# Kernel tuning notes

Hardware: AMD Instinct MI355X
Metric: run time of the kernel (lower is better)

The kernel has to match this reference:

```python
import jax, jax.numpy as jnp
import numpy as np
from jax import lax

Q = 3          # Self-ONN polynomial order
EPS = 1e-5     # InstanceNorm1d eps


def setup_inputs() -> dict:
    key = jax.random.key(0)
    k1, k2, k3 = jax.random.split(key, 3)
    B, Cin, L = 16, 128, 8192
    Cout, K = 128, 3
    x = jax.random.normal(k1, (B, Cin, L), dtype=jnp.float32)
    # Conv1d weight over power-expanded channels: [Cout, Cin*Q, K]
    W = jax.random.normal(k2, (Cout, Cin * Q, K), dtype=jnp.float32) * 0.05
    b = jax.random.normal(k3, (Cout,), dtype=jnp.float32) * 0.05
    return {"x": x, "W": W, "b": b}


def reference(x, W, b):
    x = jnp.repeat(x, 2, axis=-1)
    # Self-ONN power expansion: concat x^1..x^Q along channel dim -> (B, C*Q, 2L)
    powers = jnp.concatenate([x ** (i + 1) for i in range(Q)], axis=1)
    # Conv1d, stride 1, padding 1 (same length)
    out = lax.conv_general_dilated(
        powers, W,
        window_strides=(1,),
        padding=[(1, 1)],
        dimension_numbers=("NCH", "OIH", "NCH"),
    ) + b[None, :, None]
    # InstanceNorm1d (affine=False): normalize over length per (batch, channel)
    mean = jnp.mean(out, axis=-1, keepdims=True)
    var = jnp.var(out, axis=-1, keepdims=True)
    out = (out - mean) * lax.rsqrt(var + EPS)
    # Tanh activation (self.relu is nn.Tanh()); dropout=False -> no-op
    return jnp.tanh(out)
```

## Files before the change

kernel.cpp:

```cpp
#include <hip/hip_runtime.h>
#include <hip/hip_fp16.h>
#include <math.h>

#define BATCH 16
#define CIN   128
#define LIN   8192
#define COUT  128
#define LOUT  16384
#define KEXP  768
#define NT    128
#define NTILES (LIN/NT)
#define PCOLS 130
#define PCPAD 136
#define PSZ   (PCOLS*PCPAD)

typedef _Float16 f16x8 __attribute__((ext_vector_type(8)));
typedef float    f32x4 __attribute__((ext_vector_type(4)));

__global__ void prep_weights(const float* __restrict__ W,
                             _Float16* __restrict__ WE,
                             _Float16* __restrict__ WO) {
  int idx = blockIdx.x * 256 + threadIdx.x;
  int co = idx / KEXP;
  int k  = idx % KEXP;
  int cq = (k < 384) ? k : k - 384;
  const float* w = W + ((size_t)co * 384 + cq) * 3;
  float we, wo;
  if (k < 384) { we = w[0];        wo = w[0] + w[1]; }
  else         { we = w[1] + w[2]; wo = w[2];        }
  int mtile = co >> 4, l15 = co & 15;
  int ks = k >> 5, kk = k & 31, quad = kk >> 3, j = kk & 7;
  size_t off = ((size_t)((mtile * 24 + ks) * 64) + quad * 16 + l15) * 8 + j;
  WE[off] = (_Float16)we;
  WO[off] = (_Float16)wo;
}

__launch_bounds__(512, 2)
__global__ void conv_gemm(const float* __restrict__ x,
                          const _Float16* __restrict__ WE,
                          const _Float16* __restrict__ WO,
                          float* __restrict__ out,
                          float* __restrict__ stats) {
  extern __shared__ char smem[];
  float*    sstats = (float*)smem;
  _Float16* plane  = (_Float16*)(smem + 1024);

  const int tile = blockIdx.x;
  const int b    = blockIdx.y;
  const int i0   = tile * NT;
  const int t    = threadIdx.x;
  const int lane = t & 63;
  const int wave = t >> 6;
  const int p    = wave >> 1;
  const int isO  = wave & 1;
  const int wm   = p >> 1, wn = p & 1;
  const int l15  = lane & 15, quad = lane >> 4;

  if (t < 128) { sstats[2 * t] = 0.f; sstats[2 * t + 1] = 0.f; }

  const float* xb = x + (size_t)b * CIN * LIN;
  for (int task = t; task < PCOLS * 16; task += 512) {
    int g   = task / PCOLS;
    int col = task - g * PCOLS;
    int c8  = g * 8;
    int gi  = i0 - 1 + col;
    bool ok = (gi >= 0 && gi < LIN);
    f16x8 p1, p2, p3;
#pragma unroll
    for (int j = 0; j < 8; ++j) {
      float v = ok ? xb[(size_t)(c8 + j) * LIN + gi] : 0.f;
      float v2 = v * v;
      p1[j] = (_Float16)v;
      p2[j] = (_Float16)v2;
      p3[j] = (_Float16)(v2 * v);
    }
    _Float16* dst = plane + col * PCPAD + c8;
    *(f16x8*)(dst)           = p1;
    *(f16x8*)(dst + PSZ)     = p2;
    *(f16x8*)(dst + 2 * PSZ) = p3;
  }
  __syncthreads();

  f32x4 acc[4][4];
  const f32x4 zero = {0.f, 0.f, 0.f, 0.f};
#pragma unroll
  for (int fm = 0; fm < 4; ++fm)
#pragma unroll
    for (int fn = 0; fn < 4; ++fn) acc[fm][fn] = zero;

  const _Float16* Wsel = isO ? WO : WE;
  const int kl = quad * 8;

  f16x8 af[2][4], bf[2][4];

#define LOAD_STEP(ks_, buf_)                                                        \
  {                                                                                 \
    const int q_  = ((ks_) % 12) >> 2;                                              \
    const int cb_ = ((ks_) & 3) * 32;                                               \
    const int sh_ = ((ks_) < 12 ? 0 : 1) + isO;                                     \
    const _Float16* pb_ = plane + q_ * PSZ + cb_ + kl;                              \
    _Pragma("unroll")                                                               \
    for (int fn = 0; fn < 4; ++fn) {                                                \
      int colB = wn * 64 + fn * 16 + l15 + sh_;                                     \
      bf[buf_][fn] = *(const f16x8*)(pb_ + colB * PCPAD);                           \
    }                                                                               \
    _Pragma("unroll")                                                               \
    for (int fm = 0; fm < 4; ++fm) {                                                \
      int mt = wm * 4 + fm;                                                         \
      af[buf_][fm] = *(const f16x8*)(Wsel + ((size_t)((mt * 24 + (ks_)) * 64) + lane) * 8); \
    }                                                                               \
  }

  LOAD_STEP(0, 0)
#pragma unroll
  for (int ks = 0; ks < 24; ++ks) {
    const int cur = ks & 1, nxt = cur ^ 1;
    if (ks < 23) LOAD_STEP(ks + 1, nxt)
#pragma unroll
    for (int fm = 0; fm < 4; ++fm)
#pragma unroll
      for (int fn = 0; fn < 4; ++fn)
        acc[fm][fn] = __builtin_amdgcn_mfma_f32_16x16x32_f16(af[cur][fm], bf[cur][fn], acc[fm][fn], 0, 0, 0);
  }
#undef LOAD_STEP

  __syncthreads();
  char* ex = smem + 1024 + p * (64 * 272) + lane * 272;
  if (isO) {
#pragma unroll
    for (int fm = 0; fm < 4; ++fm)
#pragma unroll
      for (int fn = 0; fn < 4; ++fn)
        *(f32x4*)(ex + (fm * 4 + fn) * 16) = acc[fm][fn];
  }
  __syncthreads();

  if (!isO) {
    float* orow_base = out + (size_t)b * COUT * LOUT;
#pragma unroll
    for (int fm = 0; fm < 4; ++fm) {
      f32x4 accO[4];
#pragma unroll
      for (int fn = 0; fn < 4; ++fn) accO[fn] = *(f32x4*)(ex + (fm * 4 + fn) * 16);
#pragma unroll
      for (int r = 0; r < 4; ++r) {
        float s1 = 0.f, s2 = 0.f;
#pragma unroll
        for (int fn = 0; fn < 4; ++fn) {
          float vE = acc[fm][fn][r], vO = accO[fn][r];
          s1 += vE + vO;
          s2 += vE * vE + vO * vO;
        }
#pragma unroll
        for (int off = 8; off >= 1; off >>= 1) {
          s1 += __shfl_xor(s1, off, 64);
          s2 += __shfl_xor(s2, off, 64);
        }
        int co = wm * 64 + fm * 16 + quad * 4 + r;
        if (l15 == 0) {
          atomicAdd(&sstats[2 * co], s1);
          atomicAdd(&sstats[2 * co + 1], s2);
        }
        float* orow = orow_base + (size_t)co * LOUT;
#pragma unroll
        for (int fn = 0; fn < 4; ++fn) {
          int n = i0 + wn * 64 + fn * 16 + l15;
          float2 v = make_float2(acc[fm][fn][r], accO[fn][r]);
          *(float2*)(orow + 2 * n) = v;
        }
      }
    }
  }
  __syncthreads();
  if (t < 128) {
    atomicAdd(&stats[((size_t)b * COUT + t) * 2],     sstats[2 * t]);
    atomicAdd(&stats[((size_t)b * COUT + t) * 2 + 1], sstats[2 * t + 1]);
  }
}

__device__ inline float tanh_fast(float z) {
  float e = __expf(2.f * z);
  return 1.f - 2.f / (e + 1.f);
}

__global__ void norm_tanh(float* __restrict__ out, const float* __restrict__ stats) {
  int row = blockIdx.x;
  float s1 = stats[2 * row], s2 = stats[2 * row + 1];
  const float invN = 1.f / (float)LOUT;
  float mean = s1 * invN;
  float var  = fmaxf(s2 * invN - mean * mean, 0.f);
  float inv  = rsqrtf(var + 1e-5f);
  float4* p = (float4*)(out + (size_t)row * LOUT);
  for (int i = threadIdx.x; i < LOUT / 4; i += 256) {
    float4 v = p[i];
    v.x = tanh_fast((v.x - mean) * inv);
    v.y = tanh_fast((v.y - mean) * inv);
    v.z = tanh_fast((v.z - mean) * inv);
    v.w = tanh_fast((v.w - mean) * inv);
    p[i] = v;
  }
}

extern "C" void kernel_launch(void* const* d_in, const int* in_sizes, int n_in,
                              void* d_out, int out_size, void* d_ws, size_t ws_size,
                              hipStream_t stream) {
  const float* x = (const float*)d_in[0];
  const float* W = (const float*)d_in[1];
  float* out = (float*)d_out;

  float*    stats = (float*)d_ws;
  _Float16* WE    = (_Float16*)((char*)d_ws + 16384);
  _Float16* WO    = WE + (size_t)COUT * KEXP;

  hipMemsetAsync(d_ws, 0, 16384, stream);
  prep_weights<<<dim3((COUT * KEXP) / 256), dim3(256), 0, stream>>>(W, WE, WO);

  size_t shmem = 1024 + (size_t)3 * PSZ * 2;
  hipFuncSetAttribute(reinterpret_cast<const void*>(conv_gemm),
                      hipFuncAttributeMaxDynamicSharedMemorySize, (int)shmem);
  conv_gemm<<<dim3(NTILES, BATCH), dim3(512), shmem, stream>>>(x, WE, WO, out, stats);

  norm_tanh<<<dim3(BATCH * COUT), dim3(256), 0, stream>>>(out, stats);
}
```

Measured before the change: 328.5 us.

## Stream power planes one at a time to cut LDS and raise occupancy

```diff
diff --git a/kernel.cpp b/kernel.cpp
--- a/kernel.cpp
+++ b/kernel.cpp
@@ -23,19 +23,23 @@
   int idx = blockIdx.x * 256 + threadIdx.x;
   int co = idx / KEXP;
   int k  = idx % KEXP;
-  int cq = (k < 384) ? k : k - 384;
+  int sh = (k >= 384) ? 1 : 0;
+  int cq = k - 384 * sh;
   const float* w = W + ((size_t)co * 384 + cq) * 3;
   float we, wo;
-  if (k < 384) { we = w[0];        wo = w[0] + w[1]; }
+  if (sh == 0) { we = w[0];        wo = w[0] + w[1]; }
   else         { we = w[1] + w[2]; wo = w[2];        }
+  int q  = cq >> 7;
+  int c  = cq & 127;
+  int ks = q * 8 + sh * 4 + (c >> 5);
+  int kk = c & 31, quad = kk >> 3, j = kk & 7;
   int mtile = co >> 4, l15 = co & 15;
-  int ks = k >> 5, kk = k & 31, quad = kk >> 3, j = kk & 7;
   size_t off = ((size_t)((mtile * 24 + ks) * 64) + quad * 16 + l15) * 8 + j;
   WE[off] = (_Float16)we;
   WO[off] = (_Float16)wo;
 }
 
-__launch_bounds__(512, 2)
+__launch_bounds__(512, 4)
 __global__ void conv_gemm(const float* __restrict__ x,
                           const _Float16* __restrict__ WE,
                           const _Float16* __restrict__ WO,
@@ -55,31 +59,12 @@
   const int isO  = wave & 1;
   const int wm   = p >> 1, wn = p & 1;
   const int l15  = lane & 15, quad = lane >> 4;
+  const int kl   = quad * 8;
 
   if (t < 128) { sstats[2 * t] = 0.f; sstats[2 * t + 1] = 0.f; }
 
   const float* xb = x + (size_t)b * CIN * LIN;
-  for (int task = t; task < PCOLS * 16; task += 512) {
-    int g   = task / PCOLS;
-    int col = task - g * PCOLS;
-    int c8  = g * 8;
-    int gi  = i0 - 1 + col;
-    bool ok = (gi >= 0 && gi < LIN);
-    f16x8 p1, p2, p3;
-#pragma unroll
-    for (int j = 0; j < 8; ++j) {
-      float v = ok ? xb[(size_t)(c8 + j) * LIN + gi] : 0.f;
-      float v2 = v * v;
-      p1[j] = (_Float16)v;
-      p2[j] = (_Float16)v2;
-      p3[j] = (_Float16)(v2 * v);
-    }
-    _Float16* dst = plane + col * PCPAD + c8;
-    *(f16x8*)(dst)           = p1;
-    *(f16x8*)(dst + PSZ)     = p2;
-    *(f16x8*)(dst + 2 * PSZ) = p3;
-  }
-  __syncthreads();
+  const _Float16* Wsel = isO ? WO : WE;
 
   f32x4 acc[4][4];
   const f32x4 zero = {0.f, 0.f, 0.f, 0.f};
@@ -88,86 +73,77 @@
 #pragma unroll
     for (int fn = 0; fn < 4; ++fn) acc[fm][fn] = zero;
 
-  const _Float16* Wsel = isO ? WO : WE;
-  const int kl = quad * 8;
-
-  f16x8 af[2][4], bf[2][4];
-
-#define LOAD_STEP(ks_, buf_)                                                        \
-  {                                                                                 \
-    const int q_  = ((ks_) % 12) >> 2;                                              \
-    const int cb_ = ((ks_) & 3) * 32;                                               \
-    const int sh_ = ((ks_) < 12 ? 0 : 1) + isO;                                     \
-    const _Float16* pb_ = plane + q_ * PSZ + cb_ + kl;                              \
-    _Pragma("unroll")                                                               \
-    for (int fn = 0; fn < 4; ++fn) {                                                \
-      int colB = wn * 64 + fn * 16 + l15 + sh_;                                     \
-      bf[buf_][fn] = *(const f16x8*)(pb_ + colB * PCPAD);                           \
-    }                                                                               \
-    _Pragma("unroll")                                                               \
-    for (int fm = 0; fm < 4; ++fm) {                                                \
-      int mt = wm * 4 + fm;                                                         \
-      af[buf_][fm] = *(const f16x8*)(Wsel + ((size_t)((mt * 24 + (ks_)) * 64) + lane) * 8); \
-    }                                                                               \
-  }
-
-  LOAD_STEP(0, 0)
-#pragma unroll
-  for (int ks = 0; ks < 24; ++ks) {
-    const int cur = ks & 1, nxt = cur ^ 1;
-    if (ks < 23) LOAD_STEP(ks + 1, nxt)
-#pragma unroll
-    for (int fm = 0; fm < 4; ++fm)
-#pragma unroll
-      for (int fn = 0; fn < 4; ++fn)
-        acc[fm][fn] = __builtin_amdgcn_mfma_f32_16x16x32_f16(af[cur][fm], bf[cur][fn], acc[fm][fn], 0, 0, 0);
-  }
-#undef LOAD_STEP
-
-  __syncthreads();
-  char* ex = smem + 1024 + p * (64 * 272) + lane * 272;
-  if (isO) {
-#pragma unroll
-    for (int fm = 0; fm < 4; ++fm)
-#pragma unroll
-      for (int fn = 0; fn < 4; ++fn)
-        *(f32x4*)(ex + (fm * 4 + fn) * 16) = acc[fm][fn];
-  }
-  __syncthreads();
-
-  if (!isO) {
-    float* orow_base = out + (size_t)b * COUT * LOUT;
-#pragma unroll
-    for (int fm = 0; fm < 4; ++fm) {
-      f32x4 accO[4];
-#pragma unroll
-      for (int fn = 0; fn < 4; ++fn) accO[fn] = *(f32x4*)(ex + (fm * 4 + fn) * 16);
-#pragma unroll
-      for (int r = 0; r < 4; ++r) {
-        float s1 = 0.f, s2 = 0.f;
-#pragma unroll
-        for (int fn = 0; fn < 4; ++fn) {
-          float vE = acc[fm][fn][r], vO = accO[fn][r];
-          s1 += vE + vO;
-          s2 += vE * vE + vO * vO;
-        }
-#pragma unroll
-        for (int off = 8; off >= 1; off >>= 1) {
-          s1 += __shfl_xor(s1, off, 64);
-          s2 += __shfl_xor(s2, off, 64);
-        }
-        int co = wm * 64 + fm * 16 + quad * 4 + r;
-        if (l15 == 0) {
-          atomicAdd(&sstats[2 * co], s1);
-          atomicAdd(&sstats[2 * co + 1], s2);
-        }
-        float* orow = orow_base + (size_t)co * LOUT;
-#pragma unroll
-        for (int fn = 0; fn < 4; ++fn) {
-          int n = i0 + wn * 64 + fn * 16 + l15;
-          float2 v = make_float2(acc[fm][fn][r], accO[fn][r]);
-          *(float2*)(orow + 2 * n) = v;
-        }
+#pragma unroll
+  for (int q = 0; q < 3; ++q) {
+    for (int task = t; task < PCOLS * 16; task += 512) {
+      int g   = task / PCOLS;
+      int col = task - g * PCOLS;
+      int c8  = g * 8;
+      int gi  = i0 - 1 + col;
+      bool ok = (gi >= 0 && gi < LIN);
+      f16x8 w;
+#pragma unroll
+      for (int j = 0; j < 8; ++j) {
+        float v = ok ? xb[(size_t)(c8 + j) * LIN + gi] : 0.f;
+        float pv = (q == 0) ? v : ((q == 1) ? v * v : v * v * v);
+        w[j] = (_Float16)pv;
+      }
+      *(f16x8*)(plane + col * PCPAD + c8) = w;
+    }
+    __syncthreads();
+
+#pragma unroll
+    for (int s = 0; s < 8; ++s) {
+      const int cb   = (s & 3) * 32;
+      const int shft = (s >> 2) + isO;
+      const _Float16* pb = plane + cb + kl;
+      f16x8 bf[4], af[4];
+#pragma unroll
+      for (int fn = 0; fn < 4; ++fn) {
+        int colB = wn * 64 + fn * 16 + l15 + shft;
+        bf[fn] = *(const f16x8*)(pb + colB * PCPAD);
+      }
+#pragma unroll
+      for (int fm = 0; fm < 4; ++fm) {
+        int mt = wm * 4 + fm;
+        af[fm] = *(const f16x8*)(Wsel + ((size_t)((mt * 24 + q * 8 + s) * 64) + lane) * 8);
+      }
+#pragma unroll
+      for (int fm = 0; fm < 4; ++fm)
+#pragma unroll
+        for (int fn = 0; fn < 4; ++fn)
+          acc[fm][fn] = __builtin_amdgcn_mfma_f32_16x16x32_f16(af[fm], bf[fn], acc[fm][fn], 0, 0, 0);
+    }
+    __syncthreads();
+  }
+
+  float* orow_base = out + (size_t)b * COUT * LOUT + isO;
+#pragma unroll
+  for (int fm = 0; fm < 4; ++fm) {
+#pragma unroll
+    for (int r = 0; r < 4; ++r) {
+      float s1 = 0.f, s2 = 0.f;
+#pragma unroll
+      for (int fn = 0; fn < 4; ++fn) {
+        float v = acc[fm][fn][r];
+        s1 += v;
+        s2 += v * v;
+      }
+#pragma unroll
+      for (int off = 8; off >= 1; off >>= 1) {
+        s1 += __shfl_xor(s1, off, 64);
+        s2 += __shfl_xor(s2, off, 64);
+      }
+      int co = wm * 64 + fm * 16 + quad * 4 + r;
+      if (l15 == 0) {
+        atomicAdd(&sstats[2 * co], s1);
+        atomicAdd(&sstats[2 * co + 1], s2);
+      }
+      float* orow = orow_base + (size_t)co * LOUT;
+#pragma unroll
+      for (int fn = 0; fn < 4; ++fn) {
+        int n = i0 + wn * 64 + fn * 16 + l15;
+        orow[2 * n] = acc[fm][fn][r];
       }
     }
   }
@@ -180,7 +156,7 @@
 
 __device__ inline float tanh_fast(float z) {
   float e = __expf(2.f * z);
-  return 1.f - 2.f / (e + 1.f);
+  return 1.f - 2.f * __builtin_amdgcn_rcpf(e + 1.f);
 }
 
 __global__ void norm_tanh(float* __restrict__ out, const float* __restrict__ stats) {
@@ -190,13 +166,14 @@
   float mean = s1 * invN;
   float var  = fmaxf(s2 * invN - mean * mean, 0.f);
   float inv  = rsqrtf(var + 1e-5f);
+  float c0   = -mean * inv;
   float4* p = (float4*)(out + (size_t)row * LOUT);
   for (int i = threadIdx.x; i < LOUT / 4; i += 256) {
     float4 v = p[i];
-    v.x = tanh_fast((v.x - mean) * inv);
-    v.y = tanh_fast((v.y - mean) * inv);
-    v.z = tanh_fast((v.z - mean) * inv);
-    v.w = tanh_fast((v.w - mean) * inv);
+    v.x = tanh_fast(fmaf(v.x, inv, c0));
+    v.y = tanh_fast(fmaf(v.y, inv, c0));
+    v.z = tanh_fast(fmaf(v.z, inv, c0));
+    v.w = tanh_fast(fmaf(v.w, inv, c0));
     p[i] = v;
   }
 }
@@ -215,7 +192,7 @@
   hipMemsetAsync(d_ws, 0, 16384, stream);
   prep_weights<<<dim3((COUT * KEXP) / 256), dim3(256), 0, stream>>>(W, WE, WO);
 
-  size_t shmem = 1024 + (size_t)3 * PSZ * 2;
+  size_t shmem = 1024 + (size_t)PSZ * 2;
   hipFuncSetAttribute(reinterpret_cast<const void*>(conv_gemm),
                       hipFuncAttributeMaxDynamicSharedMemorySize, (int)shmem);
   conv_gemm<<<dim3(NTILES, BATCH), dim3(512), shmem, stream>>>(x, WE, WO, out, stats);
```

Result: faster. 312.2 us (-5.0%).
